# Optimization experiments

Hardware: AMD Instinct MI355X
Metric: run time of the kernel (lower is better)

The kernel has to match this reference:

```python
import jax, jax.numpy as jnp
import numpy as np

NUM_EXPERTS = 8
TOP_K = 2
HIDDEN = 2048
FFN = 4096


def setup_inputs() -> dict:
    key = jax.random.key(0)
    ks = jax.random.split(key, 5)
    s = 0.02
    return {
        "hidden_states": jax.random.normal(ks[0], (2, 2048, HIDDEN), dtype=jnp.float32),
        "w_router": jax.random.normal(ks[1], (HIDDEN, NUM_EXPERTS), dtype=jnp.float32) * s,
        "w1": jax.random.normal(ks[2], (NUM_EXPERTS, FFN, HIDDEN), dtype=jnp.float32) * s,
        "w2": jax.random.normal(ks[3], (NUM_EXPERTS, HIDDEN, FFN), dtype=jnp.float32) * s,
        "w3": jax.random.normal(ks[4], (NUM_EXPERTS, FFN, HIDDEN), dtype=jnp.float32) * s,
    }


def reference(hidden_states, w_router, w1, w2, w3):
    shape = hidden_states.shape
    x = hidden_states.reshape(-1, HIDDEN)  # [T, H]

    # Router: logits -> softmax -> top-k -> renormalize (Mixtral routing)
    logits = x @ w_router                              # [T, E]
    probs = jax.nn.softmax(logits, axis=-1)
    top_w, top_i = jax.lax.top_k(probs, TOP_K)         # [T, K]
    top_w = top_w / jnp.sum(top_w, axis=-1, keepdims=True)
    # Dense combine weights per expert: [T, E]
    combine = jnp.sum(
        jax.nn.one_hot(top_i, NUM_EXPERTS, dtype=x.dtype) * top_w[..., None], axis=1
    )

    # Grouped SwiGLU experts: out = sum_e combine[:, e] * w2_e(silu(w1_e x) * w3_e x)
    out = jnp.zeros_like(x)
    for e in range(NUM_EXPERTS):
        h = jax.nn.silu(x @ w1[e].T) * (x @ w3[e].T)   # [T, F]
        y = h @ w2[e].T                                # [T, H]
        out = out + combine[:, e:e + 1] * y

    return (out.reshape(shape), jnp.zeros((1,), dtype=x.dtype))
```

## Files before the change

### kernel.cpp

```cpp
#include <hip/hip_runtime.h>
#include <hip/hip_bf16.h>
#include <stdint.h>

#define T_TOK 4096
#define HID   2048
#define FFN_D 4096
#define NE    8
#define PADB  256

typedef __attribute__((ext_vector_type(8))) short  short8;
typedef __attribute__((ext_vector_type(4))) float  f32x4;
typedef __attribute__((ext_vector_type(4))) unsigned short u16x4;
typedef unsigned short u16;

__device__ __forceinline__ u16 f2bf(float f) {
    unsigned u = __float_as_uint(f);
    u += 0x7FFFu + ((u >> 16) & 1u);
    return (u16)(u >> 16);
}
__device__ __forceinline__ float bf2f(u16 v) {
    return __uint_as_float(((unsigned)v) << 16);
}

#define GLD16(g, l) __builtin_amdgcn_global_load_lds( \
    (const __attribute__((address_space(1))) unsigned int*)(g), \
    (__attribute__((address_space(3))) unsigned int*)(l), 16, 0, 0)

__global__ void k_convert(const float* __restrict__ s, u16* __restrict__ d, long n8) {
    for (long i = (long)blockIdx.x * 256 + threadIdx.x; i < n8; i += (long)gridDim.x * 256) {
        f32x4 a = *((const f32x4*)s + i * 2);
        f32x4 b = *((const f32x4*)s + i * 2 + 1);
        short8 o;
#pragma unroll
        for (int q = 0; q < 4; ++q) { o[q] = (short)f2bf(a[q]); o[q + 4] = (short)f2bf(b[q]); }
        *(short8*)(d + i * 8) = o;
    }
}

__global__ void k_router(const float* __restrict__ x, const float* __restrict__ wr,
                         int* __restrict__ topk_id, float* __restrict__ topk_w,
                         int* __restrict__ counts) {
    int lane = threadIdx.x & 63;
    int t = blockIdx.x * 4 + (threadIdx.x >> 6);
    const float* xr = x + (size_t)t * HID;
    float acc[8];
#pragma unroll
    for (int e = 0; e < 8; ++e) acc[e] = 0.f;
    for (int h = lane; h < HID; h += 64) {
        float xv = xr[h];
        f32x4 w0 = *(const f32x4*)(wr + h * 8);
        f32x4 w1 = *(const f32x4*)(wr + h * 8 + 4);
#pragma unroll
        for (int q = 0; q < 4; ++q) { acc[q] += xv * w0[q]; acc[4 + q] += xv * w1[q]; }
    }
#pragma unroll
    for (int e = 0; e < 8; ++e) {
        float v = acc[e];
#pragma unroll
        for (int s = 32; s > 0; s >>= 1) v += __shfl_xor(v, s);
        acc[e] = v;
    }
    if (lane == 0) {
        int i0 = 0; float l0 = acc[0];
#pragma unroll
        for (int e = 1; e < 8; ++e) if (acc[e] > l0) { l0 = acc[e]; i0 = e; }
        int i1 = -1; float l1 = -3.4e38f;
#pragma unroll
        for (int e = 0; e < 8; ++e) if (e != i0 && acc[e] > l1) { l1 = acc[e]; i1 = e; }
        float wA = 1.f / (1.f + expf(l1 - l0));
        topk_id[t * 2] = i0;  topk_id[t * 2 + 1] = i1;
        topk_w[t * 2] = wA;   topk_w[t * 2 + 1] = 1.f - wA;
        atomicAdd(&counts[i0], 1);
        atomicAdd(&counts[i1], 1);
    }
}

__global__ void k_scan(const int* __restrict__ counts, int* __restrict__ pad_off,
                       int* __restrict__ perm_tok) {
    __shared__ int sTot;
    if (threadIdx.x == 0) {
        int o = 0;
#pragma unroll
        for (int e = 0; e < 8; ++e) { pad_off[e] = o; o += ((counts[e] + PADB - 1) / PADB) * PADB; }
        pad_off[8] = o; sTot = o;
    }
    __syncthreads();
    int tot = sTot;
    for (int i = threadIdx.x; i < tot; i += 256) perm_tok[i] = 0;
}

__global__ void k_scatter(const int* __restrict__ topk_id, int* __restrict__ cursors,
                          const int* __restrict__ pad_off, int* __restrict__ perm_tok,
                          int* __restrict__ pos_of) {
    int t = blockIdx.x * 256 + threadIdx.x;
    if (t >= T_TOK) return;
#pragma unroll
    for (int k = 0; k < 2; ++k) {
        int e = topk_id[t * 2 + k];
        int p = pad_off[e] + atomicAdd(&cursors[e], 1);
        perm_tok[p] = t;
        pos_of[t * 2 + k] = p;
    }
}

template<int KTOT, int NTOT, bool DUAL, bool GATHER>
__global__ __launch_bounds__(512, 2) void k_gemm8(
    const u16* __restrict__ A,
    const u16* __restrict__ B0all,
    const u16* __restrict__ B1all,
    u16* __restrict__ C,
    const int* __restrict__ perm_tok,
    const int* __restrict__ pad_off)
{
    constexpr int BMt   = 256;
    constexpr int BNt   = DUAL ? 128 : 256;
    constexpr int NI    = DUAL ? 2 : 4;
    constexpr int NB    = NTOT / BNt;
    constexpr int CPX   = NB / 8;
    constexpr int NK    = KTOT / 64;
    constexpr int ATILE = BMt * 64;
    constexpr int BTILE = BNt * 64;
    constexpr int WCW   = DUAL ? 32 : 64;

    const int bid = blockIdx.x;
    const int xcd = bid & 7;
    const int idx = bid >> 3;
    const int m0  = (idx / CPX) * BMt;
    if (m0 >= pad_off[8]) return;
    const int n0  = (xcd * CPX + (idx % CPX)) * BNt;
    int e = 0;
    while (pad_off[e + 1] <= m0) ++e;

    __shared__ u16 As[2 * ATILE];
    __shared__ u16 Bs0[2 * BTILE];
    __shared__ u16 Bs1[DUAL ? 2 * BTILE : 8];
    __shared__ int tokS[GATHER ? BMt : 8];

    const int tid = threadIdx.x;
    const int w = tid >> 6, l = tid & 63;
    if (GATHER) {
        for (int i = tid; i < BMt; i += 512) tokS[i] = perm_tok[m0 + i];
        __syncthreads();
    }

    const u16* B0 = B0all + (size_t)e * NTOT * KTOT;
    const u16* B1 = DUAL ? (B1all + (size_t)e * NTOT * KTOT) : B0all;

    const u16* gsrc[8];
    u16* ldst[8];
    int tstep;
    {
        const int c = (l & 7) ^ (l >> 3);
#pragma unroll
        for (int j = 0; j < 8; ++j) {
            const int rl = j * 8 + (l >> 3);
            if (w < 4) {
                const int rt = w * 64 + rl;
                const long grow = GATHER ? (long)tokS[rt] : (long)(m0 + rt);
                gsrc[j] = A + grow * KTOT + c * 8;
                ldst[j] = (u16*)As + (w * 64 + j * 8) * 64;
                tstep = ATILE;
            } else if (!DUAL || w < 6) {
                const int rt = (DUAL ? ((w - 4) & 1) : (w - 4)) * 64 + rl;
                gsrc[j] = B0 + (size_t)(n0 + rt) * KTOT + c * 8;
                ldst[j] = (u16*)Bs0 + (rt - rl + j * 8) * 64;
                tstep = BTILE;
            } else {
                const int rt = ((w - 4) & 1) * 64 + rl;
                gsrc[j] = B1 + (size_t)(n0 + rt) * KTOT + c * 8;
                ldst[j] = (u16*)Bs1 + (rt - rl + j * 8) * 64;
                tstep = BTILE;
            }
        }
    }

    const int wr = w >> 2, wc = w & 3;
    const int fr = l & 15, fk = l >> 4, x7 = l & 7;
    const int pc0 = ((fk ^ x7) << 3);
    const int pc1 = pc0 ^ 32;
    const int aB = (wr * 128 + fr) * 64;
    const int bB = (wc * WCW + fr) * 64;

    f32x4 acc0[8][NI], acc1[8][NI];
    const f32x4 fz = {0.f, 0.f, 0.f, 0.f};
#pragma unroll
    for (int mi = 0; mi < 8; ++mi)
#pragma unroll
        for (int ni = 0; ni < NI; ++ni) { acc0[mi][ni] = fz; if (DUAL) acc1[mi][ni] = fz; }

#pragma unroll
    for (int j = 0; j < 8; ++j) GLD16(gsrc[j], ldst[j]);
    asm volatile("s_waitcnt vmcnt(0)" ::: "memory");
    __builtin_amdgcn_s_barrier();
    __builtin_amdgcn_sched_barrier(0);

#pragma unroll 1
    for (int t = 0; t < NK; ++t) {
        const int cb = t & 1, nb2 = cb ^ 1;
        const u16* aC  = (const u16*)As  + cb * ATILE;
        const u16* b0C = (const u16*)Bs0 + cb * BTILE;
        const u16* b1C = (const u16*)Bs1 + (DUAL ? cb * BTILE : 0);
        const long kE = (long)(t + 1) * 64;
        const bool hasNext = (t + 1 < NK);

        short8 af[4], b0f[NI], b1f[NI];

        if (hasNext) {
#pragma unroll
            for (int j = 0; j < 4; ++j) GLD16(gsrc[j] + kE, ldst[j] + nb2 * tstep);
        }
#pragma unroll
        for (int mi = 0; mi < 4; ++mi) af[mi] = *(const short8*)(aC + aB + mi * 1024 + pc0);
#pragma unroll
        for (int ni = 0; ni < NI; ++ni) {
            b0f[ni] = *(const short8*)(b0C + bB + ni * 1024 + pc0);
            if (DUAL) b1f[ni] = *(const short8*)(b1C + bB + ni * 1024 + pc0);
        }
        __builtin_amdgcn_s_setprio(1);
#pragma unroll
        for (int mi = 0; mi < 4; ++mi)
#pragma unroll
            for (int ni = 0; ni < NI; ++ni) {
                acc0[mi][ni] = __builtin_amdgcn_mfma_f32_16x16x32_bf16(af[mi], b0f[ni], acc0[mi][ni], 0, 0, 0);
                if (DUAL)
                    acc1[mi][ni] = __builtin_amdgcn_mfma_f32_16x16x32_bf16(af[mi], b1f[ni], acc1[mi][ni], 0, 0, 0);
            }
        __builtin_amdgcn_s_setprio(0);

        if (hasNext) {
#pragma unroll
            for (int j = 4; j < 8; ++j) GLD16(gsrc[j] + kE, ldst[j] + nb2 * tstep);
        }
#pragma unroll
        for (int mi = 0; mi < 4; ++mi) af[mi] = *(const short8*)(aC + aB + (mi + 4) * 1024 + pc0);
        __builtin_amdgcn_s_setprio(1);
#pragma unroll
        for (int mi = 0; mi < 4; ++mi)
#pragma unroll
            for (int ni = 0; ni < NI; ++ni) {
                acc0[mi + 4][ni] = __builtin_amdgcn_mfma_f32_16x16x32_bf16(af[mi], b0f[ni], acc0[mi + 4][ni], 0, 0, 0);
                if (DUAL)
                    acc1[mi + 4][ni] = __builtin_amdgcn_mfma_f32_16x16x32_bf16(af[mi], b1f[ni], acc1[mi + 4][ni], 0, 0, 0);
            }
        __builtin_amdgcn_s_setprio(0);

#pragma unroll
        for (int mi = 0; mi < 4; ++mi) af[mi] = *(const short8*)(aC + aB + mi * 1024 + pc1);
#pragma unroll
        for (int ni = 0; ni < NI; ++ni) {
            b0f[ni] = *(const short8*)(b0C + bB + ni * 1024 + pc1);
            if (DUAL) b1f[ni] = *(const short8*)(b1C + bB + ni * 1024 + pc1);
        }
        __builtin_amdgcn_s_setprio(1);
#pragma unroll
        for (int mi = 0; mi < 4; ++mi)
#pragma unroll
            for (int ni = 0; ni < NI; ++ni) {
                acc0[mi][ni] = __builtin_amdgcn_mfma_f32_16x16x32_bf16(af[mi], b0f[ni], acc0[mi][ni], 0, 0, 0);
                if (DUAL)
                    acc1[mi][ni] = __builtin_amdgcn_mfma_f32_16x16x32_bf16(af[mi], b1f[ni], acc1[mi][ni], 0, 0, 0);
            }
        __builtin_amdgcn_s_setprio(0);

#pragma unroll
        for (int mi = 0; mi < 4; ++mi) af[mi] = *(const short8*)(aC + aB + (mi + 4) * 1024 + pc1);
        __builtin_amdgcn_s_setprio(1);
#pragma unroll
        for (int mi = 0; mi < 4; ++mi)
#pragma unroll
            for (int ni = 0; ni < NI; ++ni) {
                acc0[mi + 4][ni] = __builtin_amdgcn_mfma_f32_16x16x32_bf16(af[mi], b0f[ni], acc0[mi + 4][ni], 0, 0, 0);
                if (DUAL)
                    acc1[mi + 4][ni] = __builtin_amdgcn_mfma_f32_16x16x32_bf16(af[mi], b1f[ni], acc1[mi + 4][ni], 0, 0, 0);
            }
        __builtin_amdgcn_s_setprio(0);

        asm volatile("s_waitcnt vmcnt(0)" ::: "memory");
        __builtin_amdgcn_s_barrier();
        __builtin_amdgcn_sched_barrier(0);
    }

    const int er = (l >> 4) * 4;
    const int ec = l & 15;
#pragma unroll
    for (int mi = 0; mi < 8; ++mi)
#pragma unroll
        for (int ni = 0; ni < NI; ++ni)
#pragma unroll
            for (int r = 0; r < 4; ++r) {
                size_t prow = (size_t)(m0 + wr * 128 + mi * 16 + er + r);
                int col = n0 + wc * WCW + ni * 16 + ec;
                float v = acc0[mi][ni][r];
                float res;
                if (DUAL) {
                    float g3 = acc1[mi][ni][r];
                    res = v / (1.f + __expf(-v)) * g3;
                } else {
                    res = v;
                }
                C[prow * NTOT + col] = f2bf(res);
            }
}

__global__ void k_combine(const u16* __restrict__ y, const int* __restrict__ pos_of,
                          const float* __restrict__ topk_w, float* __restrict__ out) {
    int idx = blockIdx.x * 256 + threadIdx.x;
    int t  = idx >> 9;
    int c4 = (idx & 511) << 2;
    int p0 = pos_of[t * 2], p1 = pos_of[t * 2 + 1];
    float w0 = topk_w[t * 2], w1 = topk_w[t * 2 + 1];
    u16x4 a = *(const u16x4*)(y + (size_t)p0 * HID + c4);
    u16x4 b = *(const u16x4*)(y + (size_t)p1 * HID + c4);
    f32x4 o;
#pragma unroll
    for (int q = 0; q < 4; ++q) o[q] = w0 * bf2f(a[q]) + w1 * bf2f(b[q]);
    *(f32x4*)(out + (size_t)t * HID + c4) = o;
    if (idx == 0) out[(size_t)T_TOK * HID] = 0.f;
}

__global__ void k_init(int* __restrict__ c) {
    if (threadIdx.x < 16) c[threadIdx.x] = 0;
}

template<int KTOT, int NTOT, bool DUAL, bool GATHER>
__global__ __launch_bounds__(256) void k_gemm_fb(
    const u16* __restrict__ A,
    const float* __restrict__ Ball0,
    const float* __restrict__ Ball1,
    u16* __restrict__ C,
    const int* __restrict__ perm_tok,
    const int* __restrict__ pad_off)
{
    const int BMf = 128;
    const int e    = blockIdx.z;
    const int base = pad_off[e];
    const int ne   = pad_off[e + 1] - base;
    const int m0   = blockIdx.y * BMf;
    if (m0 >= ne) return;
    const int n0  = blockIdx.x * 128;
    const int tid = threadIdx.x;
    const int BK = 64;

    __shared__ u16 As[128 * 64];
    __shared__ u16 Bs0[128 * 64];
    __shared__ u16 Bs1[DUAL ? 128 * 64 : 8];
    __shared__ int tokS[128];

    const float* B0 = Ball0 + (size_t)e * NTOT * KTOT;
    const float* B1 = DUAL ? (Ball1 + (size_t)e * NTOT * KTOT) : Ball0;

    if (GATHER) {
        if (tid < 128) tokS[tid] = perm_tok[base + m0 + tid];
        __syncthreads();
    }

    const int sr = tid >> 3;
    const int sc = tid & 7;
    const u16*   aRow[4];
    const float* b0Row[4];
    const float* b1Row[4];
    int dIdx[4];
#pragma unroll
    for (int i = 0; i < 4; ++i) {
        int r = sr + 32 * i;
        if (GATHER) aRow[i] = A + (size_t)tokS[r] * KTOT + sc * 8;
        else        aRow[i] = A + (size_t)(base + m0 + r) * KTOT + sc * 8;
        b0Row[i] = B0 + (size_t)(n0 + r) * KTOT + sc * 8;
        b1Row[i] = B1 + (size_t)(n0 + r) * KTOT + sc * 8;
        dIdx[i] = r * BK + ((sc ^ (sr & 7)) << 3);
    }

    const int lane = tid & 63;
    const int wid  = tid >> 6;
    const int wm   = (wid >> 1) * 64;
    const int wn   = (wid & 1) * 64;
    const int fr   = lane & 15;
    const int fk   = lane >> 4;
    const int x7   = fr & 7;

    f32x4 acc0[4][4], acc1[4][4];
    const f32x4 fz = {0.f, 0.f, 0.f, 0.f};
#pragma unroll
    for (int i = 0; i < 4; ++i)
#pragma unroll
        for (int j = 0; j < 4; ++j) { acc0[i][j] = fz; acc1[i][j] = fz; }

    for (int ks = 0; ks < KTOT / BK; ++ks) {
        short8 av[4], b0s[4], b1s[4];
#pragma unroll
        for (int i = 0; i < 4; ++i) {
            av[i] = *(const short8*)(aRow[i]);  aRow[i] += BK;
            f32x4 f0 = *(const f32x4*)(b0Row[i]);
            f32x4 f1 = *(const f32x4*)(b0Row[i] + 4);  b0Row[i] += BK;
#pragma unroll
            for (int q = 0; q < 4; ++q) { b0s[i][q] = (short)f2bf(f0[q]); b0s[i][q + 4] = (short)f2bf(f1[q]); }
            if (DUAL) {
                f32x4 g0 = *(const f32x4*)(b1Row[i]);
                f32x4 g1 = *(const f32x4*)(b1Row[i] + 4);  b1Row[i] += BK;
#pragma unroll
                for (int q = 0; q < 4; ++q) { b1s[i][q] = (short)f2bf(g0[q]); b1s[i][q + 4] = (short)f2bf(g1[q]); }
            }
        }
        __syncthreads();
#pragma unroll
        for (int i = 0; i < 4; ++i) {
            *(short8*)(&As[dIdx[i]])  = av[i];
            *(short8*)(&Bs0[dIdx[i]]) = b0s[i];
            if (DUAL) *(short8*)(&Bs1[dIdx[i]]) = b1s[i];
        }
        __syncthreads();
#pragma unroll
        for (int kk = 0; kk < 2; ++kk) {
            short8 af[4], b0f[4], b1f[4];
            const int ct = ((kk * 4 + fk) ^ x7) << 3;
#pragma unroll
            for (int i = 0; i < 4; ++i) af[i]  = *(const short8*)(&As[(wm + i * 16 + fr) * BK + ct]);
#pragma unroll
            for (int j = 0; j < 4; ++j) b0f[j] = *(const short8*)(&Bs0[(wn + j * 16 + fr) * BK + ct]);
            if (DUAL) {
#pragma unroll
                for (int j = 0; j < 4; ++j) b1f[j] = *(const short8*)(&Bs1[(wn + j * 16 + fr) * BK + ct]);
            }
#pragma unroll
            for (int i = 0; i < 4; ++i)
#pragma unroll
                for (int j = 0; j < 4; ++j) {
                    acc0[i][j] = __builtin_amdgcn_mfma_f32_16x16x32_bf16(af[i], b0f[j], acc0[i][j], 0, 0, 0);
                    if (DUAL)
                        acc1[i][j] = __builtin_amdgcn_mfma_f32_16x16x32_bf16(af[i], b1f[j], acc1[i][j], 0, 0, 0);
                }
        }
        __syncthreads();
    }

    const int er = (lane >> 4) * 4;
    const int ec = lane & 15;
#pragma unroll
    for (int i = 0; i < 4; ++i)
#pragma unroll
        for (int j = 0; j < 4; ++j)
#pragma unroll
            for (int r = 0; r < 4; ++r) {
                size_t prow = (size_t)(base + m0 + wm + i * 16 + er + r);
                int col = n0 + wn + j * 16 + ec;
                float v = acc0[i][j][r];
                float res;
                if (DUAL) {
                    float g3 = acc1[i][j][r];
                    res = v / (1.f + __expf(-v)) * g3;
                } else {
                    res = v;
                }
                C[prow * NTOT + col] = f2bf(res);
            }
}

extern "C" void kernel_launch(void* const* d_in, const int* in_sizes, int n_in,
                              void* d_out, int out_size, void* d_ws, size_t ws_size,
                              hipStream_t stream) {
    const float* x  = (const float*)d_in[0];
    const float* wr = (const float*)d_in[1];
    const float* w1 = (const float*)d_in[2];
    const float* w2 = (const float*)d_in[3];
    const float* w3 = (const float*)d_in[4];
    float* out = (float*)d_out;
    char* ws = (char*)d_ws;

    const size_t NEED = 369240064ull;

    if (ws_size >= NEED) {
        u16*  xb  = (u16*)(ws);
        u16*  wA  = (u16*)(ws + 16777216);
        u16*  w3b = (u16*)(ws + 150994944);
        u16*  hb  = (u16*)(ws + 285212672);
        u16*  yb  = (u16*)(ws + 150994944);
        int*  perm_tok = (int*)(ws + 369098752);
        int*  pos_of   = (int*)(ws + 369139712);
        int*  topk_id  = (int*)(ws + 369172480);
        float* topk_w  = (float*)(ws + 369205248);
        int*  cnt      = (int*)(ws + 369238016);
        int*  counts   = cnt;
        int*  cursors  = cnt + 8;
        int*  pad_off  = cnt + 16;

        k_init<<<1, 64, 0, stream>>>(cnt);
        k_convert<<<2048, 256, 0, stream>>>(x, xb, (long)T_TOK * HID / 8);
        k_router<<<1024, 256, 0, stream>>>(x, wr, topk_id, topk_w, counts);
        k_scan<<<1, 256, 0, stream>>>(counts, pad_off, perm_tok);
        k_scatter<<<16, 256, 0, stream>>>(topk_id, cursors, pad_off, perm_tok, pos_of);

        const long WN8 = (long)NE * FFN_D * HID / 8;
        k_convert<<<4096, 256, 0, stream>>>(w1, wA, WN8);
        k_convert<<<4096, 256, 0, stream>>>(w3, w3b, WN8);

        k_gemm8<HID, FFN_D, true, true><<<(FFN_D / 128) * 40, 512, 0, stream>>>(
            xb, wA, w3b, hb, perm_tok, pad_off);

        k_convert<<<4096, 256, 0, stream>>>(w2, wA, WN8);

        k_gemm8<FFN_D, HID, false, false><<<(HID / 256) * 40, 512, 0, stream>>>(
            hb, wA, (const u16*)nullptr, yb, perm_tok, pad_off);

        k_combine<<<8192, 256, 0, stream>>>(yb, pos_of, topk_w, out);
    } else {
        u16*  xb       = (u16*)(ws);
        u16*  hbuf     = (u16*)(ws + 16777216);
        u16*  ybuf     = (u16*)(ws + 16777216 + 83886080);
        int*  perm_tok = (int*)(ws + 16777216 + 83886080 + 41943040);
        int*  pos_of   = perm_tok + 10240;
        int*  topk_id  = pos_of + 8192;
        float* topk_w  = (float*)(topk_id + 8192);
        int*  cnt      = (int*)(topk_w + 8192);
        int*  counts   = cnt;
        int*  cursors  = cnt + 8;
        int*  pad_off  = cnt + 16;

        k_init<<<1, 64, 0, stream>>>(cnt);
        k_convert<<<2048, 256, 0, stream>>>(x, xb, (long)T_TOK * HID / 8);
        k_router<<<1024, 256, 0, stream>>>(x, wr, topk_id, topk_w, counts);
        k_scan<<<1, 256, 0, stream>>>(counts, pad_off, perm_tok);
        k_scatter<<<16, 256, 0, stream>>>(topk_id, cursors, pad_off, perm_tok, pos_of);

        k_gemm_fb<HID, FFN_D, true, true><<<dim3(FFN_D / 128, 34, NE), 256, 0, stream>>>(
            xb, w1, w3, hbuf, perm_tok, pad_off);
        k_gemm_fb<FFN_D, HID, false, false><<<dim3(HID / 128, 34, NE), 256, 0, stream>>>(
            hbuf, w2, (const float*)nullptr, ybuf, perm_tok, pad_off);

        k_combine<<<8192, 256, 0, stream>>>(ybuf, pos_of, topk_w, out);
    }
}
```

Before: 895.1 us.

## Fuse fp32-to-bf16 weight conversion into expert GEMM B-tile loads

Removes the separate weight conversion kernels for w1, w3 and w2. The grouped GEMM now reads fp32 weights straight into registers, converts them with packed bf16 conversion instructions, and writes the result to LDS, while A tiles still use direct global-to-LDS loads. The aim is to skip writing and re-reading roughly 400MB of bf16 weight copies. In exchange, the GEMM fetches twice as many weight bytes per tile and holds them in registers across the MFMA phase, which adds register pressure and VALU work inside the main loop. The small-workspace fallback path is removed.

```diff
diff --git a/kernel.cpp b/kernel.cpp
--- a/kernel.cpp
+++ b/kernel.cpp
@@ -20,6 +20,15 @@
 }
 __device__ __forceinline__ float bf2f(u16 v) {
     return __uint_as_float(((unsigned)v) << 16);
+}
+
+__device__ __forceinline__ short8 cvt8(f32x4 a, f32x4 b) {
+    union { unsigned u[4]; short8 s; } r;
+    asm("v_cvt_pk_bf16_f32 %0, %1, %2" : "=v"(r.u[0]) : "v"(a[0]), "v"(a[1]));
+    asm("v_cvt_pk_bf16_f32 %0, %1, %2" : "=v"(r.u[1]) : "v"(a[2]), "v"(a[3]));
+    asm("v_cvt_pk_bf16_f32 %0, %1, %2" : "=v"(r.u[2]) : "v"(b[0]), "v"(b[1]));
+    asm("v_cvt_pk_bf16_f32 %0, %1, %2" : "=v"(r.u[3]) : "v"(b[2]), "v"(b[3]));
+    return r.s;
 }
 
 #define GLD16(g, l) __builtin_amdgcn_global_load_lds( \
@@ -104,10 +113,10 @@
 }
 
 template<int KTOT, int NTOT, bool DUAL, bool GATHER>
-__global__ __launch_bounds__(512, 2) void k_gemm8(
+__global__ __launch_bounds__(512, 2) void k_gemm8f(
     const u16* __restrict__ A,
-    const u16* __restrict__ B0all,
-    const u16* __restrict__ B1all,
+    const float* __restrict__ B0all,
+    const float* __restrict__ B1all,
     u16* __restrict__ C,
     const int* __restrict__ perm_tok,
     const int* __restrict__ pad_off)
@@ -115,12 +124,11 @@
     constexpr int BMt   = 256;
     constexpr int BNt   = DUAL ? 128 : 256;
     constexpr int NI    = DUAL ? 2 : 4;
-    constexpr int NB    = NTOT / BNt;
-    constexpr int CPX   = NB / 8;
+    constexpr int WCW   = DUAL ? 32 : 64;
+    constexpr int CPX   = (NTOT / BNt) / 8;
     constexpr int NK    = KTOT / 64;
     constexpr int ATILE = BMt * 64;
     constexpr int BTILE = BNt * 64;
-    constexpr int WCW   = DUAL ? 32 : 64;
 
     const int bid = blockIdx.x;
     const int xcd = bid & 7;
@@ -143,35 +151,32 @@
         __syncthreads();
     }
 
-    const u16* B0 = B0all + (size_t)e * NTOT * KTOT;
-    const u16* B1 = DUAL ? (B1all + (size_t)e * NTOT * KTOT) : B0all;
-
-    const u16* gsrc[8];
-    u16* ldst[8];
-    int tstep;
-    {
-        const int c = (l & 7) ^ (l >> 3);
-#pragma unroll
-        for (int j = 0; j < 8; ++j) {
-            const int rl = j * 8 + (l >> 3);
-            if (w < 4) {
-                const int rt = w * 64 + rl;
-                const long grow = GATHER ? (long)tokS[rt] : (long)(m0 + rt);
-                gsrc[j] = A + grow * KTOT + c * 8;
-                ldst[j] = (u16*)As + (w * 64 + j * 8) * 64;
-                tstep = ATILE;
-            } else if (!DUAL || w < 6) {
-                const int rt = (DUAL ? ((w - 4) & 1) : (w - 4)) * 64 + rl;
-                gsrc[j] = B0 + (size_t)(n0 + rt) * KTOT + c * 8;
-                ldst[j] = (u16*)Bs0 + (rt - rl + j * 8) * 64;
-                tstep = BTILE;
-            } else {
-                const int rt = ((w - 4) & 1) * 64 + rl;
-                gsrc[j] = B1 + (size_t)(n0 + rt) * KTOT + c * 8;
-                ldst[j] = (u16*)Bs1 + (rt - rl + j * 8) * 64;
-                tstep = BTILE;
-            }
-        }
+    const float* B0 = B0all + (size_t)e * NTOT * KTOT;
+    const float* B1 = DUAL ? (B1all + (size_t)e * NTOT * KTOT) : B0all;
+
+    const int lr = l >> 3;
+    const int c  = (l & 7) ^ lr;
+
+    const u16* aSrc[4];
+    u16* aDst[4];
+#pragma unroll
+    for (int ja = 0; ja < 4; ++ja) {
+        const int row = w * 32 + ja * 8 + lr;
+        const long ar = GATHER ? (long)tokS[row] : (long)(m0 + row);
+        aSrc[ja] = A + ar * KTOT + c * 8;
+        aDst[ja] = (u16*)As + (w * 32 + ja * 8) * 64;
+    }
+
+    const float* Bg = DUAL ? (w < 4 ? B0 : B1) : B0;
+    u16* bL = DUAL ? (w < 4 ? (u16*)Bs0 : (u16*)Bs1) : (u16*)Bs0;
+    const int bBase = DUAL ? (w & 3) * 32 : w * 32;
+    const float* bSrc[4];
+    u16* bDst[4];
+#pragma unroll
+    for (int jb = 0; jb < 4; ++jb) {
+        const int rowb = bBase + jb * 8 + lr;
+        bSrc[jb] = Bg + (size_t)(n0 + rowb) * KTOT + c * 8;
+        bDst[jb] = bL + (bBase + jb * 8) * 64 + l * 8;
     }
 
     const int wr = w >> 2, wc = w & 3;
@@ -188,27 +193,45 @@
 #pragma unroll
         for (int ni = 0; ni < NI; ++ni) { acc0[mi][ni] = fz; if (DUAL) acc1[mi][ni] = fz; }
 
-#pragma unroll
-    for (int j = 0; j < 8; ++j) GLD16(gsrc[j], ldst[j]);
-    asm volatile("s_waitcnt vmcnt(0)" ::: "memory");
+    f32x4 br[8];
+
+#pragma unroll
+    for (int jb = 0; jb < 4; ++jb) {
+        br[2 * jb]     = ((const f32x4*)bSrc[jb])[0];
+        br[2 * jb + 1] = ((const f32x4*)bSrc[jb])[1];
+    }
+#pragma unroll
+    for (int ja = 0; ja < 4; ++ja) GLD16(aSrc[ja], aDst[ja]);
+#pragma unroll
+    for (int jb = 0; jb < 4; ++jb)
+        *(short8*)(bDst[jb]) = cvt8(br[2 * jb], br[2 * jb + 1]);
+    asm volatile("s_waitcnt vmcnt(0) lgkmcnt(0)" ::: "memory");
     __builtin_amdgcn_s_barrier();
     __builtin_amdgcn_sched_barrier(0);
 
 #pragma unroll 1
     for (int t = 0; t < NK; ++t) {
-        const int cb = t & 1, nb2 = cb ^ 1;
+        const int cb = t & 1, nb = cb ^ 1;
+        const long kE = (long)(t + 1) * 64;
+        const bool hasNext = (t + 1 < NK);
         const u16* aC  = (const u16*)As  + cb * ATILE;
         const u16* b0C = (const u16*)Bs0 + cb * BTILE;
         const u16* b1C = (const u16*)Bs1 + (DUAL ? cb * BTILE : 0);
-        const long kE = (long)(t + 1) * 64;
-        const bool hasNext = (t + 1 < NK);
+
+        if (hasNext) {
+#pragma unroll
+            for (int jb = 0; jb < 4; ++jb) {
+                const f32x4* p = (const f32x4*)(bSrc[jb] + kE);
+                br[2 * jb]     = p[0];
+                br[2 * jb + 1] = p[1];
+            }
+#pragma unroll
+            for (int ja = 0; ja < 4; ++ja) GLD16(aSrc[ja] + kE, aDst[ja] + nb * ATILE);
+        }
+        __builtin_amdgcn_sched_barrier(0);
 
         short8 af[4], b0f[NI], b1f[NI];
 
-        if (hasNext) {
-#pragma unroll
-            for (int j = 0; j < 4; ++j) GLD16(gsrc[j] + kE, ldst[j] + nb2 * tstep);
-        }
 #pragma unroll
         for (int mi = 0; mi < 4; ++mi) af[mi] = *(const short8*)(aC + aB + mi * 1024 + pc0);
 #pragma unroll
@@ -227,10 +250,6 @@
             }
         __builtin_amdgcn_s_setprio(0);
 
-        if (hasNext) {
-#pragma unroll
-            for (int j = 4; j < 8; ++j) GLD16(gsrc[j] + kE, ldst[j] + nb2 * tstep);
-        }
 #pragma unroll
         for (int mi = 0; mi < 4; ++mi) af[mi] = *(const short8*)(aC + aB + (mi + 4) * 1024 + pc0);
         __builtin_amdgcn_s_setprio(1);
@@ -274,8 +293,15 @@
                     acc1[mi + 4][ni] = __builtin_amdgcn_mfma_f32_16x16x32_bf16(af[mi], b1f[ni], acc1[mi + 4][ni], 0, 0, 0);
             }
         __builtin_amdgcn_s_setprio(0);
-
-        asm volatile("s_waitcnt vmcnt(0)" ::: "memory");
+        __builtin_amdgcn_sched_barrier(0);
+
+        if (hasNext) {
+#pragma unroll
+            for (int jb = 0; jb < 4; ++jb)
+                *(short8*)(bDst[jb] + nb * BTILE) = cvt8(br[2 * jb], br[2 * jb + 1]);
+        }
+
+        asm volatile("s_waitcnt vmcnt(0) lgkmcnt(0)" ::: "memory");
         __builtin_amdgcn_s_barrier();
         __builtin_amdgcn_sched_barrier(0);
     }
@@ -322,139 +348,6 @@
     if (threadIdx.x < 16) c[threadIdx.x] = 0;
 }
 
-template<int KTOT, int NTOT, bool DUAL, bool GATHER>
-__global__ __launch_bounds__(256) void k_gemm_fb(
-    const u16* __restrict__ A,
-    const float* __restrict__ Ball0,
-    const float* __restrict__ Ball1,
-    u16* __restrict__ C,
-    const int* __restrict__ perm_tok,
-    const int* __restrict__ pad_off)
-{
-    const int BMf = 128;
-    const int e    = blockIdx.z;
-    const int base = pad_off[e];
-    const int ne   = pad_off[e + 1] - base;
-    const int m0   = blockIdx.y * BMf;
-    if (m0 >= ne) return;
-    const int n0  = blockIdx.x * 128;
-    const int tid = threadIdx.x;
-    const int BK = 64;
-
-    __shared__ u16 As[128 * 64];
-    __shared__ u16 Bs0[128 * 64];
-    __shared__ u16 Bs1[DUAL ? 128 * 64 : 8];
-    __shared__ int tokS[128];
-
-    const float* B0 = Ball0 + (size_t)e * NTOT * KTOT;
-    const float* B1 = DUAL ? (Ball1 + (size_t)e * NTOT * KTOT) : Ball0;
-
-    if (GATHER) {
-        if (tid < 128) tokS[tid] = perm_tok[base + m0 + tid];
-        __syncthreads();
-    }
-
-    const int sr = tid >> 3;
-    const int sc = tid & 7;
-    const u16*   aRow[4];
-    const float* b0Row[4];
-    const float* b1Row[4];
-    int dIdx[4];
-#pragma unroll
-    for (int i = 0; i < 4; ++i) {
-        int r = sr + 32 * i;
-        if (GATHER) aRow[i] = A + (size_t)tokS[r] * KTOT + sc * 8;
-        else        aRow[i] = A + (size_t)(base + m0 + r) * KTOT + sc * 8;
-        b0Row[i] = B0 + (size_t)(n0 + r) * KTOT + sc * 8;
-        b1Row[i] = B1 + (size_t)(n0 + r) * KTOT + sc * 8;
-        dIdx[i] = r * BK + ((sc ^ (sr & 7)) << 3);
-    }
-
-    const int lane = tid & 63;
-    const int wid  = tid >> 6;
-    const int wm   = (wid >> 1) * 64;
-    const int wn   = (wid & 1) * 64;
-    const int fr   = lane & 15;
-    const int fk   = lane >> 4;
-    const int x7   = fr & 7;
-
-    f32x4 acc0[4][4], acc1[4][4];
-    const f32x4 fz = {0.f, 0.f, 0.f, 0.f};
-#pragma unroll
-    for (int i = 0; i < 4; ++i)
-#pragma unroll
-        for (int j = 0; j < 4; ++j) { acc0[i][j] = fz; acc1[i][j] = fz; }
-
-    for (int ks = 0; ks < KTOT / BK; ++ks) {
-        short8 av[4], b0s[4], b1s[4];
-#pragma unroll
-        for (int i = 0; i < 4; ++i) {
-            av[i] = *(const short8*)(aRow[i]);  aRow[i] += BK;
-            f32x4 f0 = *(const f32x4*)(b0Row[i]);
-            f32x4 f1 = *(const f32x4*)(b0Row[i] + 4);  b0Row[i] += BK;
-#pragma unroll
-            for (int q = 0; q < 4; ++q) { b0s[i][q] = (short)f2bf(f0[q]); b0s[i][q + 4] = (short)f2bf(f1[q]); }
-            if (DUAL) {
-                f32x4 g0 = *(const f32x4*)(b1Row[i]);
-                f32x4 g1 = *(const f32x4*)(b1Row[i] + 4);  b1Row[i] += BK;
-#pragma unroll
-                for (int q = 0; q < 4; ++q) { b1s[i][q] = (short)f2bf(g0[q]); b1s[i][q + 4] = (short)f2bf(g1[q]); }
-            }
-        }
-        __syncthreads();
-#pragma unroll
-        for (int i = 0; i < 4; ++i) {
-            *(short8*)(&As[dIdx[i]])  = av[i];
-            *(short8*)(&Bs0[dIdx[i]]) = b0s[i];
-            if (DUAL) *(short8*)(&Bs1[dIdx[i]]) = b1s[i];
-        }
-        __syncthreads();
-#pragma unroll
-        for (int kk = 0; kk < 2; ++kk) {
-            short8 af[4], b0f[4], b1f[4];
-            const int ct = ((kk * 4 + fk) ^ x7) << 3;
-#pragma unroll
-            for (int i = 0; i < 4; ++i) af[i]  = *(const short8*)(&As[(wm + i * 16 + fr) * BK + ct]);
-#pragma unroll
-            for (int j = 0; j < 4; ++j) b0f[j] = *(const short8*)(&Bs0[(wn + j * 16 + fr) * BK + ct]);
-            if (DUAL) {
-#pragma unroll
-                for (int j = 0; j < 4; ++j) b1f[j] = *(const short8*)(&Bs1[(wn + j * 16 + fr) * BK + ct]);
-            }
-#pragma unroll
-            for (int i = 0; i < 4; ++i)
-#pragma unroll
-                for (int j = 0; j < 4; ++j) {
-                    acc0[i][j] = __builtin_amdgcn_mfma_f32_16x16x32_bf16(af[i], b0f[j], acc0[i][j], 0, 0, 0);
-                    if (DUAL)
-                        acc1[i][j] = __builtin_amdgcn_mfma_f32_16x16x32_bf16(af[i], b1f[j], acc1[i][j], 0, 0, 0);
-                }
-        }
-        __syncthreads();
-    }
-
-    const int er = (lane >> 4) * 4;
-    const int ec = lane & 15;
-#pragma unroll
-    for (int i = 0; i < 4; ++i)
-#pragma unroll
-        for (int j = 0; j < 4; ++j)
-#pragma unroll
-            for (int r = 0; r < 4; ++r) {
-                size_t prow = (size_t)(base + m0 + wm + i * 16 + er + r);
-                int col = n0 + wn + j * 16 + ec;
-                float v = acc0[i][j][r];
-                float res;
-                if (DUAL) {
-                    float g3 = acc1[i][j][r];
-                    res = v / (1.f + __expf(-v)) * g3;
-                } else {
-                    res = v;
-                }
-                C[prow * NTOT + col] = f2bf(res);
-            }
-}
-
 extern "C" void kernel_launch(void* const* d_in, const int* in_sizes, int n_in,
                               void* d_out, int out_size, void* d_ws, size_t ws_size,
                               hipStream_t stream) {
@@ -466,66 +359,29 @@
     float* out = (float*)d_out;
     char* ws = (char*)d_ws;
 
-    const size_t NEED = 369240064ull;
-
-    if (ws_size >= NEED) {
-        u16*  xb  = (u16*)(ws);
-        u16*  wA  = (u16*)(ws + 16777216);
-        u16*  w3b = (u16*)(ws + 150994944);
-        u16*  hb  = (u16*)(ws + 285212672);
-        u16*  yb  = (u16*)(ws + 150994944);
-        int*  perm_tok = (int*)(ws + 369098752);
-        int*  pos_of   = (int*)(ws + 369139712);
-        int*  topk_id  = (int*)(ws + 369172480);
-        float* topk_w  = (float*)(ws + 369205248);
-        int*  cnt      = (int*)(ws + 369238016);
-        int*  counts   = cnt;
-        int*  cursors  = cnt + 8;
-        int*  pad_off  = cnt + 16;
-
-        k_init<<<1, 64, 0, stream>>>(cnt);
-        k_convert<<<2048, 256, 0, stream>>>(x, xb, (long)T_TOK * HID / 8);
-        k_router<<<1024, 256, 0, stream>>>(x, wr, topk_id, topk_w, counts);
-        k_scan<<<1, 256, 0, stream>>>(counts, pad_off, perm_tok);
-        k_scatter<<<16, 256, 0, stream>>>(topk_id, cursors, pad_off, perm_tok, pos_of);
-
-        const long WN8 = (long)NE * FFN_D * HID / 8;
-        k_convert<<<4096, 256, 0, stream>>>(w1, wA, WN8);
-        k_convert<<<4096, 256, 0, stream>>>(w3, w3b, WN8);
-
-        k_gemm8<HID, FFN_D, true, true><<<(FFN_D / 128) * 40, 512, 0, stream>>>(
-            xb, wA, w3b, hb, perm_tok, pad_off);
-
-        k_convert<<<4096, 256, 0, stream>>>(w2, wA, WN8);
-
-        k_gemm8<FFN_D, HID, false, false><<<(HID / 256) * 40, 512, 0, stream>>>(
-            hb, wA, (const u16*)nullptr, yb, perm_tok, pad_off);
-
-        k_combine<<<8192, 256, 0, stream>>>(yb, pos_of, topk_w, out);
-    } else {
-        u16*  xb       = (u16*)(ws);
-        u16*  hbuf     = (u16*)(ws + 16777216);
-        u16*  ybuf     = (u16*)(ws + 16777216 + 83886080);
-        int*  perm_tok = (int*)(ws + 16777216 + 83886080 + 41943040);
-        int*  pos_of   = perm_tok + 10240;
-        int*  topk_id  = pos_of + 8192;
-        float* topk_w  = (float*)(topk_id + 8192);
-        int*  cnt      = (int*)(topk_w + 8192);
-        int*  counts   = cnt;
-        int*  cursors  = cnt + 8;
-        int*  pad_off  = cnt + 16;
-
-        k_init<<<1, 64, 0, stream>>>(cnt);
-        k_convert<<<2048, 256, 0, stream>>>(x, xb, (long)T_TOK * HID / 8);
-        k_router<<<1024, 256, 0, stream>>>(x, wr, topk_id, topk_w, counts);
-        k_scan<<<1, 256, 0, stream>>>(counts, pad_off, perm_tok);
-        k_scatter<<<16, 256, 0, stream>>>(topk_id, cursors, pad_off, perm_tok, pos_of);
-
-        k_gemm_fb<HID, FFN_D, true, true><<<dim3(FFN_D / 128, 34, NE), 256, 0, stream>>>(
-            xb, w1, w3, hbuf, perm_tok, pad_off);
-        k_gemm_fb<FFN_D, HID, false, false><<<dim3(HID / 128, 34, NE), 256, 0, stream>>>(
-            hbuf, w2, (const float*)nullptr, ybuf, perm_tok, pad_off);
-
-        k_combine<<<8192, 256, 0, stream>>>(ybuf, pos_of, topk_w, out);
-    }
-}
+    u16*  xb  = (u16*)(ws);
+    u16*  hb  = (u16*)(ws + 16777216);
+    u16*  yb  = (u16*)(ws + 100663296);
+    int*  perm_tok = (int*)(ws + 142606336);
+    int*  pos_of   = (int*)(ws + 142647296);
+    int*  topk_id  = (int*)(ws + 142680064);
+    float* topk_w  = (float*)(ws + 142712832);
+    int*  cnt      = (int*)(ws + 142745600);
+    int*  counts   = cnt;
+    int*  cursors  = cnt + 8;
+    int*  pad_off  = cnt + 16;
+
+    k_init<<<1, 64, 0, stream>>>(cnt);
+    k_convert<<<2048, 256, 0, stream>>>(x, xb, (long)T_TOK * HID / 8);
+    k_router<<<1024, 256, 0, stream>>>(x, wr, topk_id, topk_w, counts);
+    k_scan<<<1, 256, 0, stream>>>(counts, pad_off, perm_tok);
+    k_scatter<<<16, 256, 0, stream>>>(topk_id, cursors, pad_off, perm_tok, pos_of);
+
+    k_gemm8f<HID, FFN_D, true, true><<<(FFN_D / 128) * 40, 512, 0, stream>>>(
+        xb, w1, w3, hb, perm_tok, pad_off);
+
+    k_gemm8f<FFN_D, HID, false, false><<<(HID / 256) * 40, 512, 0, stream>>>(
+        hb, w2, (const float*)nullptr, yb, perm_tok, pad_off);
+
+    k_combine<<<8192, 256, 0, stream>>>(yb, pos_of, topk_w, out);
+}
```

Result: slower. 1.010 ms (median of 2 runs) (+12.8%).
